# Performance work log

Measured on AMD Instinct MI355X. Metric: run time of the kernel, lower is better.

The kernel has to match this reference:

```python
import jax, jax.numpy as jnp
import numpy as np

B, L, N, C = 32, 12, 512, 2
UNITS, OUT_DIM, HORIZON, K, NUM_LAYERS = 64, 1, 12, 2, 2
M = 2 * K + 1  # 2 supports * K diffusion steps + identity


def _random_walk(adj):
    # adj: (B, N, N); D^-1 (adj + I)
    adj = adj + jnp.eye(adj.shape[1], dtype=adj.dtype)[None]
    d_inv = 1.0 / jnp.sum(adj, axis=2)
    d_inv = jnp.where(jnp.isinf(d_inv), 0.0, d_inv)
    return d_inv[:, :, None] * adj  # diag(d_inv) @ adj


def _gconv(x_in, state, supports, W, b):
    # x_in: (B, N*in), state: (B, N*units) -> (B, N*out)
    b_sz = x_in.shape[0]
    x = jnp.concatenate([x_in.reshape(b_sz, N, -1), state.reshape(b_sz, N, -1)], axis=2)
    f = x.shape[2]
    x0 = x
    xs = [x0]
    for A in supports:
        x1 = jnp.einsum('bij,bjf->bif', A, x0)
        xs.append(x1)
        for _ in range(2, K + 1):
            x2 = 2.0 * jnp.einsum('bij,bjf->bif', A, x1) - x0
            xs.append(x2)
            x1, x0 = x2, x1  # faithful to original code (x0 carries across supports)
    xcat = jnp.stack(xs, axis=0)              # (M, B, N, f)
    xcat = xcat.transpose(1, 2, 3, 0).reshape(b_sz * N, f * M)
    out = xcat @ W + b
    return out.reshape(b_sz, N * W.shape[1])


def _cell(inp, hx, supports, p):
    Wg, bg, Wc, bc = p
    gate = jax.nn.sigmoid(_gconv(inp, hx, supports, Wg, bg)).reshape(-1, N, 2 * UNITS)
    r = gate[..., :UNITS].reshape(-1, N * UNITS)
    u = gate[..., UNITS:].reshape(-1, N * UNITS)
    c = jnp.tanh(_gconv(inp, r * hx, supports, Wc, bc))
    return u * hx + (1.0 - u) * c


def setup_inputs() -> dict:
    key = jax.random.key(0)
    ks = iter(jax.random.split(key, 32))
    def nrm(shape, scale=0.1):
        return jax.random.normal(next(ks), shape, dtype=jnp.float32) * scale
    inp = {
        'history_data': jax.random.normal(next(ks), (B, L, N, C), dtype=jnp.float32),
        'hidden_states': jax.random.normal(next(ks), (B, N, 96), dtype=jnp.float32),
        'sampled_adj': jax.random.uniform(next(ks), (B, N, N), dtype=jnp.float32),
    }
    sizes = {'enc0': C + UNITS, 'enc1': 2 * UNITS, 'dec0': OUT_DIM + UNITS, 'dec1': 2 * UNITS}
    for name, isz in sizes.items():
        inp[name + '_Wg'] = nrm((isz * M, 2 * UNITS))
        inp[name + '_bg'] = jnp.ones((2 * UNITS,), jnp.float32)   # bias_start=1.0
        inp[name + '_Wc'] = nrm((isz * M, UNITS))
        inp[name + '_bc'] = jnp.zeros((UNITS,), jnp.float32)
    inp['proj_W'] = nrm((UNITS, OUT_DIM))
    inp['proj_b'] = jnp.zeros((OUT_DIM,), jnp.float32)
    inp['fc1_W'] = nrm((96, 256))
    inp['fc1_b'] = jnp.zeros((256,), jnp.float32)
    inp['fc2_W'] = nrm((256, 64))
    inp['fc2_b'] = jnp.zeros((64,), jnp.float32)
    return inp


def _forward(history_data, hidden_states, sampled_adj,
             enc0_Wg, enc0_bg, enc0_Wc, enc0_bc, enc1_Wg, enc1_bg, enc1_Wc, enc1_bc,
             dec0_Wg, dec0_bg, dec0_Wc, dec0_bc, dec1_Wg, dec1_bg, dec1_Wc, dec1_bc,
             proj_W, proj_b, fc1_W, fc1_b, fc2_W, fc2_b):
    supports = [_random_walk(sampled_adj), _random_walk(jnp.swapaxes(sampled_adj, -1, -2))]
    enc_params = [(enc0_Wg, enc0_bg, enc0_Wc, enc0_bc), (enc1_Wg, enc1_bg, enc1_Wc, enc1_bc)]
    dec_params = [(dec0_Wg, dec0_bg, dec0_Wc, dec0_bc), (dec1_Wg, dec1_bg, dec1_Wc, dec1_bc)]

    hist = jnp.transpose(history_data.reshape(B, L, N * C), (1, 0, 2))  # (L, B, N*C)

    def enc_step(h, x_t):
        out = x_t
        new_h = []
        for i, p in enumerate(enc_params):
            nh = _cell(out, h[i], supports, p)
            new_h.append(nh)
            out = nh
        return jnp.stack(new_h), None

    h0 = jnp.zeros((NUM_LAYERS, B, N * UNITS), dtype=hist.dtype)
    enc_h, _ = jax.lax.scan(enc_step, h0, hist)

    # fc_his on TSFormer hidden states, added to every encoder layer's hidden
    his = jax.nn.relu(jax.nn.relu(hidden_states @ fc1_W + fc1_b) @ fc2_W + fc2_b)  # (B, N, 64)
    enc_h = (enc_h.reshape(NUM_LAYERS, B, N, UNITS) + his[None]).reshape(NUM_LAYERS, B, N * UNITS)

    go = jnp.zeros((B, N * OUT_DIM), dtype=hist.dtype)

    def dec_step(carry, _):
        dec_in, h = carry
        out = dec_in
        new_h = []
        for i, p in enumerate(dec_params):
            nh = _cell(out, h[i], supports, p)
            new_h.append(nh)
            out = nh
        proj = (out.reshape(-1, UNITS) @ proj_W + proj_b).reshape(B, N * OUT_DIM)
        return (proj, jnp.stack(new_h)), proj

    _, outs = jax.lax.scan(dec_step, (go, enc_h), None, length=HORIZON)  # (L, B, N*OUT)
    return jnp.transpose(outs, (1, 2, 0))  # (B, N*OUT_DIM, HORIZON)


def reference(history_data, hidden_states, sampled_adj,
              enc0_Wg, enc0_bg, enc0_Wc, enc0_bc, enc1_Wg, enc1_bg, enc1_Wc, enc1_bc,
              dec0_Wg, dec0_bg, dec0_Wc, dec0_bc, dec1_Wg, dec1_bg, dec1_Wc, dec1_bc,
              proj_W, proj_b, fc1_W, fc1_b, fc2_W, fc2_b):
    return _forward(history_data, hidden_states, sampled_adj,
                    enc0_Wg, enc0_bg, enc0_Wc, enc0_bc, enc1_Wg, enc1_bg, enc1_Wc, enc1_bc,
                    dec0_Wg, dec0_bg, dec0_Wc, dec0_bc, dec1_Wg, dec1_bg, dec1_Wc, dec1_bc,
                    proj_W, proj_b, fc1_W, fc1_b, fc2_W, fc2_b)
```

## Files before the change

### kernel.cpp

```cpp
#include <hip/hip_runtime.h>
#include <stdint.h>
#include <string.h>
#include <math.h>


using bfrag = __attribute__((__ext_vector_type__(8))) short;
using accv  = __attribute__((__ext_vector_type__(4))) float;

#define DEVI static __device__ __forceinline__

DEVI float bf2f(short x) {
  union { unsigned u; float f; } v; v.u = ((unsigned)(unsigned short)x) << 16; return v.f;
}
DEVI short f2bf(float f) {
  union { float f; unsigned u; } v; v.f = f;
  unsigned r = v.u + 0x7FFFu + ((v.u >> 16) & 1u);
  return (short)(r >> 16);
}
DEVI float ldx(const void* p, long i, int f32) {
  return f32 ? ((const float*)p)[i] : bf2f(((const short*)p)[i]);
}
DEVI void gl16(const short* g, short* l) {
  __builtin_amdgcn_global_load_lds(
      (const __attribute__((address_space(1))) void*)g,
      (__attribute__((address_space(3))) void*)l, 16, 0, 0);
}
template<int N> DEVI void s_wait_vmcnt() {
  asm volatile("s_waitcnt vmcnt(%0)" :: "i"(N) : "memory");
}

struct GP {
  const short* A;  long sA;  int lda;
  const short* BT; long sBT; int ldbt;
  int K;
  short* C; long sC; int ldc;
  short* CT;
  const void* bias;
  const short* V0;
  const int* flg;
  int outDim, oshift;
  int mtiles;
  const float* h; float* hw; const float* u;
  short* xc; int inpOff;
  short* xgs; int xgsOff;
  short* xch;
  short* nxg; short* nxc;
  const void* hsrc; long hoff;
  const void* prw; const void* prb; void* dout; int tstep;
  short* xo0; short* xo1;
};

template<int EPI, int BM, int BN, int BK, int THR, int SWZ, int PIPE, int PAIR = 0>
__global__ __launch_bounds__(THR)
void gemm_k(GP pa, GP pb) {
  constexpr int W    = THR / 64;
  constexpr int WROW = BM / 32;
  constexpr int WCOL = (W / WROW < 1) ? 1 : W / WROW;
  constexpr int NT   = BN / (16 * WCOL);
  constexpr int CH   = BK / 8;
  constexpr int AI   = (BM * CH) / THR;
  constexpr int BI   = (BN * CH) / THR;
  constexpr int LD   = AI + BI;
  constexpr int TB   = (BM + BN) * BK;
  __shared__ __align__(16) short lds[PIPE*TB];
  const int tid  = threadIdx.x;
  const int w    = tid >> 6;
  const int lane = tid & 63;
  const int quad = lane >> 4, l16 = lane & 15;
  const int rowW = (w % WROW) * 32;
  const int colW = (w / WROW) * (NT * 16);
  int lay = 0;
  if constexpr (PAIR) lay = blockIdx.z;
  const GP& p = lay ? pb : pa;
  int m0, n0, bz;
  if constexpr (SWZ == 1) {
    const int blk = blockIdx.x;
    bz = blk & 31;
    const int tile = blk >> 5;
    m0 = (tile % p.mtiles) * BM;
    n0 = (tile / p.mtiles) * BN;
  } else {
    m0 = blockIdx.x * BM; n0 = blockIdx.y * BN;
    bz = PAIR ? 0 : blockIdx.z;
  }

  const short* Ab = p.A  + (long)bz * p.sA + m0 * (long)p.lda;
  const short* Bb = p.BT + (long)bz * p.sBT + n0 * (long)p.ldbt;

  accv acc[2][NT];
#pragma unroll
  for (int i = 0; i < 2; i++)
#pragma unroll
    for (int j = 0; j < NT; j++) { accv z = {0.f,0.f,0.f,0.f}; acc[i][j] = z; }

  const short* asrc[AI]; int aoff[AI];
#pragma unroll
  for (int i = 0; i < AI; i++) {
    const int s = (w*AI + i)*64 + lane;
    const int r = s / CH, c = (s % CH) ^ (r & 7);
    asrc[i] = Ab + (long)r * p.lda + c*8;
    aoff[i] = (w*AI + i)*512;
  }
  const short* bsrc[BI]; int boff[BI];
#pragma unroll
  for (int i = 0; i < BI; i++) {
    const int s = (w*BI + i)*64 + lane;
    const int r = s / CH, c = (s % CH) ^ (r & 7);
    bsrc[i] = Bb + (long)r * p.ldbt + c*8;
    boff[i] = BM*BK + (w*BI + i)*512;
  }

  const int nIter = p.K / BK;
#pragma unroll
  for (int s = 0; s < PIPE-1; ++s) {
    if (s < nIter) {
      const int kk = s * BK;
#pragma unroll
      for (int i = 0; i < AI; i++) gl16(asrc[i] + kk, &lds[s*TB + aoff[i]]);
#pragma unroll
      for (int i = 0; i < BI; i++) gl16(bsrc[i] + kk, &lds[s*TB + boff[i]]);
    }
  }

  for (int it = 0; it < nIter; ++it) {
    const int bufO = (it & (PIPE-1)) * TB;
    if (it + PIPE - 1 < nIter) {
      const int nxt = ((it + PIPE - 1) & (PIPE-1)) * TB;
      const int kk = (it + PIPE - 1) * BK;
#pragma unroll
      for (int i = 0; i < AI; i++) gl16(asrc[i] + kk, &lds[nxt + aoff[i]]);
#pragma unroll
      for (int i = 0; i < BI; i++) gl16(bsrc[i] + kk, &lds[nxt + boff[i]]);
    }
    const int rem = nIter - 1 - it;
    if (rem >= PIPE-1) { s_wait_vmcnt<(PIPE-1)*LD>(); }
    else {
      if constexpr (PIPE >= 8) { if (rem == 6) s_wait_vmcnt<6*LD>(); }
      if constexpr (PIPE >= 7) { if (rem == 5) s_wait_vmcnt<5*LD>(); }
      if constexpr (PIPE >= 6) { if (rem == 4) s_wait_vmcnt<4*LD>(); }
      if constexpr (PIPE >= 5) { if (rem == 3) s_wait_vmcnt<3*LD>(); }
      if constexpr (PIPE >= 4) { if (rem == 2) s_wait_vmcnt<2*LD>(); }
      if (rem == 1) s_wait_vmcnt<1*LD>();
      else if (rem == 0) s_wait_vmcnt<0>();
    }
    asm volatile("s_barrier" ::: "memory");
#pragma unroll
    for (int ks = 0; ks < BK; ks += 32) {
      const int ch = (ks >> 3) + quad;
      bfrag fa[2];
#pragma unroll
      for (int rt = 0; rt < 2; rt++) {
        const int ar = rowW + rt*16 + l16;
        fa[rt] = *(const bfrag*)&lds[bufO + (ar*CH + (ch ^ (ar & 7))) * 8];
      }
#pragma unroll
      for (int nt = 0; nt < NT; nt++) {
        const int br = colW + nt*16 + l16;
        bfrag fb = *(const bfrag*)&lds[bufO + BM*BK + (br*CH + (ch ^ (br & 7))) * 8];
        acc[0][nt] = __builtin_amdgcn_mfma_f32_16x16x32_bf16(fa[0], fb, acc[0][nt], 0, 0, 0);
        acc[1][nt] = __builtin_amdgcn_mfma_f32_16x16x32_bf16(fa[1], fb, acc[1][nt], 0, 0, 0);
      }
    }
    asm volatile("s_barrier" ::: "memory");
  }

  int f32 = 0;
  if constexpr (EPI == 1 || EPI == 4 || EPI == 5) f32 = *p.flg;

  if constexpr (EPI == 0 || EPI == 1 || EPI == 2) {
#pragma unroll
    for (int rt = 0; rt < 2; rt++) {
      const int rbase = m0 + rowW + rt*16 + quad*4;
#pragma unroll
      for (int nt = 0; nt < NT; nt++) {
        const int cc = n0 + colW + nt*16 + l16;
#pragma unroll
        for (int e = 0; e < 4; e++) {
          float val = acc[rt][nt][e];
          if constexpr (EPI == 1) { val += ldx(p.bias, cc, f32); val = val > 0.f ? val : 0.f; }
          p.C[(long)bz * p.sC + (long)(rbase + e) * p.ldc + cc] = f2bf(val);
        }
      }
    }
  }
  if constexpr (EPI == 2 || EPI == 3) {
    __syncthreads();
#pragma unroll
    for (int rt = 0; rt < 2; rt++)
#pragma unroll
      for (int nt = 0; nt < NT; nt++)
#pragma unroll
        for (int e = 0; e < 4; e++)
          lds[(colW + nt*16 + l16)*136 + (rowW + rt*16 + quad*4 + e)] = f2bf(acc[rt][nt][e]);
    __syncthreads();
    const int c = tid >> 2, seg = tid & 3;
    const int cG = n0 + c;
    const short* sp = &lds[c*136 + seg*32];
    long dst;
    if constexpr (EPI == 3) {
      const int m  = cG >> p.oshift;
      const int o  = cG & (p.outDim - 1);
      const int bb = m0 >> 9;
      dst = ((long)((bb * p.outDim + o) * 5 + m) << 9) + (m0 & 511) + seg*32;
    } else {
      dst = (((long)bz << 9) + cG) * 512 + m0 + seg*32;
    }
    short* dp = p.CT + dst;
    *(bfrag*)(dp)      = *(const bfrag*)(sp);
    *(bfrag*)(dp + 8)  = *(const bfrag*)(sp + 8);
    *(bfrag*)(dp + 16) = *(const bfrag*)(sp + 16);
    *(bfrag*)(dp + 24) = *(const bfrag*)(sp + 24);
  }
  if constexpr (EPI == 4) {
#pragma unroll
    for (int rt = 0; rt < 2; rt++) {
      const int nb = m0 + rowW + rt*16 + quad*4;
#pragma unroll
      for (int nt = 0; nt < NT; nt++) {
        const int o = n0 + colW + nt*16 + l16;
        const float bv = ldx(p.bias, o, f32);
#pragma unroll
        for (int e = 0; e < 4; e++) {
          const int nn = nb + e;
          float val = acc[rt][nt][e] + bv +
                      bf2f(p.V0[(long)(bz * p.outDim + o) * 2560 + nn]);
          const float s = 1.f / (1.f + __expf(-val));
          const long bn = ((long)bz << 9) + nn;
          if (o < 64) p.xc[bn*128 + p.inpOff + o] = f2bf(s * p.h[(bn << 6) + o]);
          else        p.hw[(bn << 6) + (o - 64)] = s;
        }
      }
    }
  }
  if constexpr (EPI == 5) {
    float pacc[2][4] = {};
    float pwv[NT] = {};
    const bool doproj = (p.dout != nullptr);
    if (doproj) {
#pragma unroll
      for (int nt = 0; nt < NT; nt++) pwv[nt] = ldx(p.prw, colW + nt*16 + l16, f32);
    }
#pragma unroll
    for (int rt = 0; rt < 2; rt++) {
      const int nb = m0 + rowW + rt*16 + quad*4;
#pragma unroll
      for (int nt = 0; nt < NT; nt++) {
        const int o = n0 + colW + nt*16 + l16;
        const float bv = ldx(p.bias, o, f32);
#pragma unroll
        for (int e = 0; e < 4; e++) {
          const int nn = nb + e;
          float val = acc[rt][nt][e] + bv +
                      bf2f(p.V0[(long)(bz * p.outDim + o) * 2560 + nn]);
          const float cth = tanhf(val);
          const long bn = ((long)bz << 9) + nn;
          const long idx = bn*64 + o;
          const float uo = p.u[idx];
          const float hn = uo * p.h[idx] + (1.f - uo) * cth;
          p.hw[idx] = hn;
          pacc[rt][e] += hn * pwv[nt];
          const short hb = f2bf(hn);
          if (p.xgs) p.xgs[bn*128 + p.xgsOff + o] = hb;
          if (p.nxg) { p.nxg[bn*128 + o] = hb; p.nxc[bn*128 + o] = hb; }
          if (p.hsrc != nullptr && o < 2) {
            const short hv = f2bf(ldx(p.hsrc, p.hoff + (long)bz*12288 + (long)nn*2 + o, f32));
            p.xgs[bn*128 + o] = hv;
            p.xch[bn*128 + o] = hv;
          }
        }
      }
    }
    if (doproj) {
      __syncthreads();
      float* fl = (float*)lds;
#pragma unroll
      for (int rt = 0; rt < 2; rt++)
#pragma unroll
        for (int e = 0; e < 4; e++) {
          float v = pacc[rt][e];
          v += __shfl_xor(v, 1, 16);
          v += __shfl_xor(v, 2, 16);
          v += __shfl_xor(v, 4, 16);
          v += __shfl_xor(v, 8, 16);
          if (l16 == 0) fl[(rowW + rt*16 + quad*4 + e) * WCOL + (w / WROW)] = v;
        }
      __syncthreads();
      if (tid < BM) {
        float s = ldx(p.prb, 0, f32);
#pragma unroll
        for (int g = 0; g < WCOL; g++) s += fl[tid*WCOL + g];
        const long row = ((long)bz << 9) + m0 + tid;
        if (f32) ((float*)p.dout)[row*12 + p.tstep] = s;
        else     ((short*)p.dout)[row*12 + p.tstep] = f2bf(s);
        const short ob = f2bf(s);
        p.xo0[row*128] = ob;
        p.xo1[row*128] = ob;
      }
    }
  }
}


__global__ void detect_k(const short* bg0, int* flag) {
  if (threadIdx.x == 0 && blockIdx.x == 0)
    *flag = (bg0[0] == (short)0x3F80) ? 0 : 1;
}

__global__ void rowsum_inv(const void* adj, const int* flg, float* rsi) {
  const int f32 = *flg;
  const int wid  = (blockIdx.x * 256 + threadIdx.x) >> 6;
  const int lane = threadIdx.x & 63;
  const long base = (long)wid * 512;
  float s = 0.f;
  for (int j = lane; j < 512; j += 64) s += ldx(adj, base + j, f32);
  for (int off = 32; off > 0; off >>= 1) s += __shfl_down(s, off, 64);
  if (lane == 0) rsi[wid] = 1.f / (1.f + s);
}

__global__ void colsum_inv(const void* adj, const int* flg, float* csi) {
  const int f32 = *flg;
  const int i = blockIdx.x * 256 + threadIdx.x;
  const int b = i >> 9, col = i & 511;
  const long base = (long)b * 262144 + col;
  float s = 1.f;
  for (int j = 0; j < 512; j++) s += ldx(adj, base + (long)j * 512, f32);
  csi[i] = 1.f / s;
}

__global__ __launch_bounds__(256)
void build_a(const void* adj, const int* flg, const float* rsi, const float* csi,
             short* Pbig, short* A1T, short* A2) {
  const int f32 = *flg;
  __shared__ __align__(16) float t[64 * 65];
  const int b = blockIdx.z, ti = blockIdx.x, tj = blockIdx.y;
  const int tid = threadIdx.x;
  const int r = tid >> 2, cs = (tid & 3) * 16;
  const long base = (long)b * 262144 + (long)(ti*64 + r) * 512 + tj*64 + cs;
#pragma unroll
  for (int j = 0; j < 16; j++) t[r*65 + cs + j] = ldx(adj, base + j, f32);
  __syncthreads();
  {
    const int gi = ti*64 + r;
    const float inv = rsi[b*512 + gi];
    short o[16];
#pragma unroll
    for (int j = 0; j < 16; j++) {
      const int gj = tj*64 + cs + j;
      o[j] = f2bf((t[r*65 + cs + j] + (gi == gj ? 1.f : 0.f)) * inv);
    }
    short* dp = Pbig + ((long)(b*512 + gi) << 11) + tj*64 + cs;
    bfrag v0 = {o[0],o[1],o[2],o[3],o[4],o[5],o[6],o[7]};
    bfrag v1 = {o[8],o[9],o[10],o[11],o[12],o[13],o[14],o[15]};
    *(bfrag*)dp = v0; *(bfrag*)(dp + 8) = v1;
  }
  {
    const int y = tj*64 + r;
    const float invc = csi[b*512 + y];
    short o1[16], o2[16];
#pragma unroll
    for (int j = 0; j < 16; j++) {
      const int x = ti*64 + cs + j;
      const float av = t[(cs + j)*65 + r];
      const float d = (x == y) ? 1.f : 0.f;
      o1[j] = f2bf((av + d) * rsi[b*512 + x]);
      o2[j] = f2bf((av + d) * invc);
    }
    short* d1 = A1T + ((long)(b*512 + y) << 9) + ti*64 + cs;
    short* d2 = A2  + ((long)(b*512 + y) << 9) + ti*64 + cs;
    bfrag a0 = {o1[0],o1[1],o1[2],o1[3],o1[4],o1[5],o1[6],o1[7]};
    bfrag a1 = {o1[8],o1[9],o1[10],o1[11],o1[12],o1[13],o1[14],o1[15]};
    bfrag b0 = {o2[0],o2[1],o2[2],o2[3],o2[4],o2[5],o2[6],o2[7]};
    bfrag b1 = {o2[8],o2[9],o2[10],o2[11],o2[12],o2[13],o2[14],o2[15]};
    *(bfrag*)d1 = a0; *(bfrag*)(d1 + 8) = a1;
    *(bfrag*)d2 = b0; *(bfrag*)(d2 + 8) = b1;
  }
}

__global__ void build_wcat(const void* W, const int* flg, short* WT, int f, int out) {
  const int f32 = *flg;
  const int i = blockIdx.x * 256 + threadIdx.x;
  if (i >= 5 * out * 128) return;
  const int feat = i & 127;
  const int mo = i >> 7;
  const int m = mo / out;
  const int o = mo - m * out;
  float v = 0.f;
  if (feat < f) {
    const long base = (long)feat * 5 * out;
    const float w0 = ldx(W, base + 0*out + o, f32);
    const float w1 = ldx(W, base + 1*out + o, f32);
    const float w2 = ldx(W, base + 2*out + o, f32);
    const float w3 = ldx(W, base + 3*out + o, f32);
    const float w4 = ldx(W, base + 4*out + o, f32);
    v = (m == 0) ? (w0 - w2) : (m == 1) ? (w1 - w4) : (m == 2) ? 2.f*w2
      : (m == 3) ? w3 : 2.f*w4;
  }
  WT[(long)mo * 128 + feat] = f2bf(v);
}

__global__ void build_fc1T(const void* W, const int* flg, short* WT) {
  const int f32 = *flg;
  const int i = blockIdx.x * 256 + threadIdx.x;
  const int o = i >> 7, k = i & 127;
  WT[i] = (k < 96) ? f2bf(ldx(W, (long)k*256 + o, f32)) : (short)0;
}
__global__ void build_fc2T(const void* W, const int* flg, short* WT) {
  const int f32 = *flg;
  const int i = blockIdx.x * 256 + threadIdx.x;
  const int o = i >> 8, k = i & 255;
  WT[i] = f2bf(ldx(W, (long)k*64 + o, f32));
}
__global__ void pack_hid(const void* hd, const int* flg, short* hp) {
  const int f32 = *flg;
  const int i = blockIdx.x * 256 + threadIdx.x;
  const int row = i >> 7, k = i & 127;
  hp[i] = (k < 96) ? f2bf(ldx(hd, (long)row*96 + k, f32)) : (short)0;
}

__global__ void seed_hist(const void* hist, const int* flg, short* Xg0, short* Xc0) {
  const int f32 = *flg;
  const int i = blockIdx.x * 256 + threadIdx.x;
  const int row = i >> 1, c = i & 1;
  const short v = f2bf(ldx(hist, (long)(row >> 9)*12288 + (long)(row & 511)*2 + c, f32));
  Xg0[(long)row*128 + c] = v;
  Xc0[(long)row*128 + c] = v;
}

__global__ void his_add(float* h0, float* h1, const short* his,
                        short* Xg0, short* Xc0, short* Xg1) {
  const int i = blockIdx.x * 256 + threadIdx.x;
  const int row = i >> 6, o = i & 63;
  const float v = bf2f(his[i]);
  const float a = h0[i] + v, b = h1[i] + v;
  h0[i] = a; h1[i] = b;
  Xg0[(long)row*128 + 1 + o]  = f2bf(a);
  Xg1[(long)row*128 + 64 + o] = f2bf(b);
  if (o == 0) { Xg0[(long)row*128] = 0; Xc0[(long)row*128] = 0; }
}

extern "C" void kernel_launch(void* const* d_in, const int* in_sizes, int n_in,
                              void* d_out, int out_size, void* d_ws, size_t ws_size,
                              hipStream_t stream) {
  (void)in_sizes; (void)n_in; (void)out_size;
  const void* hist   = d_in[0];
  const void* hidden = d_in[1];
  const void* adj    = d_in[2];
  const void* Wg[4] = {d_in[3], d_in[7],  d_in[11], d_in[15]};
  const void* bg[4] = {d_in[4], d_in[8],  d_in[12], d_in[16]};
  const void* Wc[4] = {d_in[5], d_in[9],  d_in[13], d_in[17]};
  const void* bc[4] = {d_in[6], d_in[10], d_in[14], d_in[18]};
  const void* projW = d_in[19];
  const void* projb = d_in[20];
  const void* fc1W  = d_in[21];
  const void* fc1b  = d_in[22];
  const void* fc2W  = d_in[23];
  const void* fc2b  = d_in[24];

  char* wp = (char*)d_ws;
  auto alloc = [&](size_t bytes) { char* r = wp; wp += (bytes + 255) & ~(size_t)255; return r; };
  short* Pbig = (short*)alloc(32ull*512*2048*2);
  float* ub   = (float*)alloc(16384ull*64*4);
  float* h0   = (float*)alloc(16384ull*64*4);
  float* h1   = (float*)alloc(16384ull*64*4);
  short* hisb = (short*)alloc(16384ull*64*2);
  short* wctg[4]; for (int i = 0; i < 4; i++) wctg[i] = (short*)alloc(640*128*2);
  short* wctc[4]; for (int i = 0; i < 4; i++) wctc[i] = (short*)alloc(320*128*2);
  float* rsi = (float*)alloc(16384*4);
  float* csi = (float*)alloc(16384*4);
  int*   flg = (int*)alloc(256);
  char* ubase = wp;
  short* hidp = (short*)ubase;
  short* mid  = (short*)(ubase + 4194304);
  short* fc1T = (short*)(ubase + 4194304 + 8388608);
  short* fc2T = (short*)(ubase + 4194304 + 8388608 + 65536);
  short* A1T  = (short*)ubase;
  short* A2   = (short*)(ubase + 16777216);
  short* P3T  = (short*)(ubase + 33554432);
  short* VTg0 = (short*)ubase;
  short* VTc0 = (short*)(ubase + 20971520);
  short* Xg0  = (short*)(ubase + 31457280);
  short* Xc0  = (short*)(ubase + 35651584);
  short* Xg1a = (short*)(ubase + 39845888);
  short* Xc1a = (short*)(ubase + 44040192);
  short* VTg1 = (short*)(ubase + 50331648);
  short* VTc1 = (short*)(ubase + 71303168);
  short* Xg1b = (short*)(ubase + 81788928);
  short* Xc1b = (short*)(ubase + 85983232);
  float* ub1  = (float*)(ubase + 90177536);
  const size_t need_serial = (size_t)(ubase - (char*)d_ws) + 50331648;
  const size_t need_pip    = (size_t)(ubase - (char*)d_ws) + 94371840;
  if (ws_size < need_serial) return;
  const bool pip = (ws_size >= need_pip);

  detect_k<<<1, 64, 0, stream>>>((const short*)bg[0], flg);
  hipMemsetAsync(h0, 0, 16384ull*64*4, stream);
  hipMemsetAsync(h1, 0, 16384ull*64*4, stream);

  const int fdim[4] = {66, 128, 65, 128};
  for (int i = 0; i < 4; i++) {
    build_wcat<<<320, 256, 0, stream>>>(Wg[i], flg, wctg[i], fdim[i], 128);
    build_wcat<<<160, 256, 0, stream>>>(Wc[i], flg, wctc[i], fdim[i], 64);
  }
  build_fc1T<<<128, 256, 0, stream>>>(fc1W, flg, fc1T);
  build_fc2T<<<64, 256, 0, stream>>>(fc2W, flg, fc2T);
  pack_hid<<<8192, 256, 0, stream>>>(hidden, flg, hidp);

  GP p;
  p = GP{}; p.A = hidp; p.lda = 128; p.BT = fc1T; p.ldbt = 128; p.K = 128;
  p.C = mid; p.ldc = 256; p.bias = fc1b; p.flg = flg;
  gemm_k<1,128,64,64,256,0,2><<<dim3(128, 4, 1), 256, 0, stream>>>(p, p);
  p = GP{}; p.A = mid; p.lda = 256; p.BT = fc2T; p.ldbt = 256; p.K = 256;
  p.C = hisb; p.ldc = 64; p.bias = fc2b; p.flg = flg;
  gemm_k<1,128,64,64,256,0,2><<<dim3(128, 1, 1), 256, 0, stream>>>(p, p);

  rowsum_inv<<<4096, 256, 0, stream>>>(adj, flg, rsi);
  colsum_inv<<<64, 256, 0, stream>>>(adj, flg, csi);
  build_a<<<dim3(8, 8, 32), 256, 0, stream>>>(adj, flg, rsi, csi, Pbig, A1T, A2);

  p = GP{}; p.A = Pbig; p.sA = 512*2048; p.lda = 2048;
  p.BT = A1T; p.sBT = 512*512; p.ldbt = 512; p.K = 512;
  p.C = Pbig + 512; p.sC = 512*2048; p.ldc = 2048; p.flg = flg;
  gemm_k<0,128,64,64,256,0,2><<<dim3(4, 8, 32), 256, 0, stream>>>(p, p);
  p = GP{}; p.A = A2; p.sA = 512*512; p.lda = 512;
  p.BT = A1T; p.sBT = 512*512; p.ldbt = 512; p.K = 512;
  p.C = Pbig + 1024; p.sC = 512*2048; p.ldc = 2048; p.CT = P3T; p.flg = flg;
  gemm_k<2,128,64,64,256,0,2><<<dim3(4, 8, 32), 256, 0, stream>>>(p, p);
  p = GP{}; p.A = A2; p.sA = 512*512; p.lda = 512;
  p.BT = P3T; p.sBT = 512*512; p.ldbt = 512; p.K = 512;
  p.C = Pbig + 1536; p.sC = 512*2048; p.ldc = 2048; p.flg = flg;
  gemm_k<0,128,64,64,256,0,2><<<dim3(4, 8, 32), 256, 0, stream>>>(p, p);

  hipMemsetAsync(Xg0, 0, 4ull*4194304, stream);
  seed_hist<<<128, 256, 0, stream>>>(hist, flg, Xg0, Xc0);

  auto run_cell = [&](int wi, int inpOff, float* hstate, short* XgL, short* XcL,
                      short* nxg, short* nxc, const void* hsrc, long hoff,
                      short* vtg, short* vtc, float* ubuf, void* dout, int tstep) {
    GP q;
    q = GP{}; q.A = XgL; q.lda = 128; q.BT = wctg[wi]; q.ldbt = 128; q.K = 128;
    q.CT = vtg; q.outDim = 128; q.oshift = 7; q.flg = flg;
    gemm_k<3,128,128,64,512,0,2><<<dim3(128, 5, 1), 512, 0, stream>>>(q, q);
    q = GP{}; q.A = Pbig; q.sA = 512*2048; q.lda = 2048;
    q.BT = vtg + 512; q.sBT = 128*2560; q.ldbt = 2560; q.K = 2048;
    q.V0 = vtg; q.outDim = 128; q.bias = bg[wi]; q.flg = flg; q.mtiles = 8;
    q.h = hstate; q.hw = ubuf; q.xc = XcL; q.inpOff = inpOff;
    gemm_k<4,64,64,64,256,1,4><<<dim3(512, 1, 1), 256, 0, stream>>>(q, q);
    q = GP{}; q.A = XcL; q.lda = 128; q.BT = wctc[wi]; q.ldbt = 128; q.K = 128;
    q.CT = vtc; q.outDim = 64; q.oshift = 6; q.flg = flg;
    gemm_k<3,128,64,64,256,0,2><<<dim3(128, 5, 1), 256, 0, stream>>>(q, q);
    q = GP{}; q.A = Pbig; q.sA = 512*2048; q.lda = 2048;
    q.BT = vtc + 512; q.sBT = 64*2560; q.ldbt = 2560; q.K = 2048;
    q.V0 = vtc; q.outDim = 64; q.bias = bc[wi]; q.flg = flg; q.mtiles = 16;
    q.h = hstate; q.hw = hstate; q.u = ubuf;
    q.xgs = XgL; q.xgsOff = inpOff; q.xch = XcL;
    q.nxg = nxg; q.nxc = nxc; q.hsrc = hsrc; q.hoff = hoff;
    q.prw = projW; q.prb = projb; q.dout = dout; q.tstep = tstep;
    q.xo0 = Xg0; q.xo1 = Xc0;
    gemm_k<5,32,64,64,256,1,4><<<dim3(512, 1, 1), 256, 0, stream>>>(q, q);
  };

  if (pip) {
    run_cell(0, 2, h0, Xg0, Xc0, Xg1a, Xc1a, hist, 1024, VTg0, VTc0, ub, nullptr, 0);
    for (int s = 1; s <= 11; s++) {
      short* XgR = ((s-1) & 1) ? Xg1b : Xg1a;
      short* XcR = ((s-1) & 1) ? Xc1b : Xc1a;
      short* XgW = (s & 1) ? Xg1b : Xg1a;
      short* XcW = (s & 1) ? Xc1b : Xc1a;
      GP qa, qb;
      qa = GP{}; qa.A = Xg0; qa.lda = 128; qa.BT = wctg[0]; qa.ldbt = 128; qa.K = 128;
      qa.CT = VTg0; qa.outDim = 128; qa.oshift = 7; qa.flg = flg;
      qb = qa; qb.A = XgR; qb.BT = wctg[1]; qb.CT = VTg1;
      gemm_k<3,128,128,64,512,0,2,1><<<dim3(128, 5, 2), 512, 0, stream>>>(qa, qb);
      qa = GP{}; qa.A = Pbig; qa.sA = 512*2048; qa.lda = 2048;
      qa.BT = VTg0 + 512; qa.sBT = 128*2560; qa.ldbt = 2560; qa.K = 2048;
      qa.V0 = VTg0; qa.outDim = 128; qa.bias = bg[0]; qa.flg = flg; qa.mtiles = 8;
      qa.h = h0; qa.hw = ub; qa.xc = Xc0; qa.inpOff = 2;
      qb = qa; qb.BT = VTg1 + 512; qb.V0 = VTg1; qb.bias = bg[1];
      qb.h = h1; qb.hw = ub1; qb.xc = XcR; qb.inpOff = 64;
      gemm_k<4,64,128,64,512,1,2,1><<<dim3(256, 1, 2), 512, 0, stream>>>(qa, qb);
      qa = GP{}; qa.A = Xc0; qa.lda = 128; qa.BT = wctc[0]; qa.ldbt = 128; qa.K = 128;
      qa.CT = VTc0; qa.outDim = 64; qa.oshift = 6; qa.flg = flg;
      qb = qa; qb.A = XcR; qb.BT = wctc[1]; qb.CT = VTc1;
      gemm_k<3,128,64,64,256,0,2,1><<<dim3(128, 5, 2), 256, 0, stream>>>(qa, qb);
      qa = GP{}; qa.A = Pbig; qa.sA = 512*2048; qa.lda = 2048;
      qa.BT = VTc0 + 512; qa.sBT = 64*2560; qa.ldbt = 2560; qa.K = 2048;
      qa.V0 = VTc0; qa.outDim = 64; qa.bias = bc[0]; qa.flg = flg; qa.mtiles = 8;
      qa.h = h0; qa.hw = h0; qa.u = ub;
      qa.xgs = Xg0; qa.xgsOff = 2; qa.xch = Xc0;
      qa.nxg = XgW; qa.nxc = XcW;
      qa.hsrc = (s < 11) ? hist : nullptr; qa.hoff = (long)(s + 1) * 1024;
      qb = qa; qb.BT = VTc1 + 512; qb.V0 = VTc1; qb.bias = bc[1];
      qb.h = h1; qb.hw = h1; qb.u = ub1;
      qb.xgs = XgW; qb.xgsOff = 64; qb.xch = nullptr;
      qb.nxg = nullptr; qb.nxc = nullptr; qb.hsrc = nullptr; qb.hoff = 0;
      gemm_k<5,64,64,64,256,1,4,1><<<dim3(256, 1, 2), 256, 0, stream>>>(qa, qb);
    }
    run_cell(1, 64, h1, Xg1b, Xc1b, nullptr, nullptr, nullptr, 0, VTg1, VTc1, ub1,
             nullptr, 0);
  } else {
    for (int t = 0; t < 12; t++) {
      run_cell(0, 2, h0, Xg0, Xc0, Xg1a, Xc1a,
               (t < 11) ? hist : nullptr, (long)(t + 1) * 1024, VTg0, VTc0, ub, nullptr, 0);
      run_cell(1, 64, h1, Xg1a, Xc1a, nullptr, nullptr, nullptr, 0, VTg0, VTc0, ub,
               nullptr, 0);
    }
  }

  his_add<<<4096, 256, 0, stream>>>(h0, h1, hisb, Xg0, Xc0, Xg1a);

  for (int t = 0; t < 12; t++) {
    run_cell(2, 1, h0, Xg0, Xc0, Xg1a, Xc1a, nullptr, 0, VTg0, VTc0, ub, nullptr, 0);
    run_cell(3, 64, h1, Xg1a, Xc1a, nullptr, nullptr, nullptr, 0, VTg0, VTc0, ub,
             d_out, t);
  }
}
```

Before: 3.145 ms.

## Fuse candidate weight projection into gate GEMM epilogue; parallelize column sums

The gate GEMM epilogue (EPI 4) now takes the freshly written r*h tile of Xc, loads the candidate weight matrix into LDS and computes the Xc·Wc projection itself, writing VTc directly. This removes the separate EPI 3 candidate projection launch each step, along with the global round-trip before it. The tile-to-block mapping is changed so that one of each pair of n-tiles owns a full row block. The column-sum kernel is also split into a partial-sum kernel with atomics plus a small inversion kernel, which gives more parallelism than the old per-column serial loop. In exchange, the epilogue does extra serialized work in only half of the gate blocks, and the atomics make the column sums nondeterministic in order.

Result: faster. 3.060 ms (-2.7%).

```diff
diff --git a/kernel.cpp b/kernel.cpp
--- a/kernel.cpp
+++ b/kernel.cpp
@@ -42,6 +42,7 @@
   int mtiles;
   const float* h; float* hw; const float* u;
   short* xc; int inpOff;
+  const short* wct; short* vtcout;
   short* xgs; int xgsOff;
   short* xch;
   short* nxg; short* nxc;
@@ -77,8 +78,12 @@
     const int blk = blockIdx.x;
     bz = blk & 31;
     const int tile = blk >> 5;
-    m0 = (tile % p.mtiles) * BM;
-    n0 = (tile / p.mtiles) * BN;
+    if (EPI == 4 && p.wct != nullptr && BN == 64) {
+      m0 = (tile >> 1) * BM; n0 = (tile & 1) * BN;
+    } else {
+      m0 = (tile % p.mtiles) * BM;
+      n0 = (tile / p.mtiles) * BN;
+    }
   } else {
     m0 = blockIdx.x * BM; n0 = blockIdx.y * BN;
     bz = PAIR ? 0 : blockIdx.z;
@@ -229,6 +234,68 @@
           if (o < 64) p.xc[bn*128 + p.inpOff + o] = f2bf(s * p.h[(bn << 6) + o]);
           else        p.hw[(bn << 6) + (o - 64)] = s;
         }
+      }
+    }
+    if (p.wct != nullptr && (BN == 128 || n0 == 0)) {
+      s_wait_vmcnt<0>();
+      __syncthreads();
+      constexpr int AG2 = 16 / W;
+      {
+        const short* xrow = p.xc + ((long)bz*512 + m0)*128;
+#pragma unroll
+        for (int i = 0; i < AG2; i++) {
+          const int s = (w*AG2 + i)*64 + lane;
+          const int r = s >> 4, c = (s & 15) ^ (r & 7);
+          gl16(xrow + (long)r*128 + c*8, &lds[(w*AG2 + i)*512]);
+        }
+      }
+      constexpr int CW2 = W / 2;
+      constexpr int NT2 = 64 / (16 * CW2);
+      const int colW2 = (w >> 1) * (NT2 * 16);
+      const int rowW2 = (w & 1) * 32;
+      for (int ncb = 0; ncb < 5; ncb++) {
+#pragma unroll
+        for (int i = 0; i < AG2; i++) {
+          const int s = (w*AG2 + i)*64 + lane;
+          const int j = s >> 4, c = (s & 15) ^ (j & 7);
+          const int cc = ncb*64 + j;
+          const int mo = (cc % 5)*64 + cc/5;
+          gl16(p.wct + (long)mo*128 + c*8, &lds[8192 + (w*AG2 + i)*512]);
+        }
+        s_wait_vmcnt<0>();
+        asm volatile("s_barrier" ::: "memory");
+        accv a2[2][NT2];
+#pragma unroll
+        for (int i2 = 0; i2 < 2; i2++)
+#pragma unroll
+          for (int j2 = 0; j2 < NT2; j2++) { accv z = {0.f,0.f,0.f,0.f}; a2[i2][j2] = z; }
+#pragma unroll
+        for (int k4 = 0; k4 < 4; k4++) {
+          bfrag fa2[2];
+#pragma unroll
+          for (int rt = 0; rt < 2; rt++) {
+            const int ar = rowW2 + rt*16 + l16;
+            fa2[rt] = *(const bfrag*)&lds[(ar*16 + ((k4*4 + quad) ^ (ar & 7)))*8];
+          }
+#pragma unroll
+          for (int nt = 0; nt < NT2; nt++) {
+            const int jb = colW2 + nt*16 + l16;
+            bfrag fb2 = *(const bfrag*)&lds[8192 + (jb*16 + ((k4*4 + quad) ^ (jb & 7)))*8];
+            a2[0][nt] = __builtin_amdgcn_mfma_f32_16x16x32_bf16(fa2[0], fb2, a2[0][nt], 0, 0, 0);
+            a2[1][nt] = __builtin_amdgcn_mfma_f32_16x16x32_bf16(fa2[1], fb2, a2[1][nt], 0, 0, 0);
+          }
+        }
+#pragma unroll
+        for (int rt = 0; rt < 2; rt++)
+#pragma unroll
+          for (int nt = 0; nt < NT2; nt++) {
+            const int cc = ncb*64 + colW2 + nt*16 + l16;
+            const long cbase = (((long)(bz*320 + cc)) << 9) + m0 + rowW2 + rt*16 + quad*4;
+#pragma unroll
+            for (int e = 0; e < 4; e++)
+              p.vtcout[cbase + e] = f2bf(a2[rt][nt][e]);
+          }
+        asm volatile("s_barrier" ::: "memory");
       }
     }
   }
@@ -317,14 +384,22 @@
   if (lane == 0) rsi[wid] = 1.f / (1.f + s);
 }
 
-__global__ void colsum_inv(const void* adj, const int* flg, float* csi) {
-  const int f32 = *flg;
+__global__ void colsum_part(const void* adj, const int* flg, float* csum) {
+  const int f32 = *flg;
+  const int b = blockIdx.x >> 4, rc = blockIdx.x & 15;
+  const int col = threadIdx.x;
+  float s0 = 0.f, s1 = 0.f;
+  const long base = (long)b * 262144 + (long)rc * 32 * 512;
+  for (int r = 0; r < 32; r++) {
+    s0 += ldx(adj, base + (long)r*512 + col, f32);
+    s1 += ldx(adj, base + (long)r*512 + col + 256, f32);
+  }
+  atomicAdd(&csum[b*512 + col], s0);
+  atomicAdd(&csum[b*512 + col + 256], s1);
+}
+__global__ void inv1p(float* v) {
   const int i = blockIdx.x * 256 + threadIdx.x;
-  const int b = i >> 9, col = i & 511;
-  const long base = (long)b * 262144 + col;
-  float s = 1.f;
-  for (int j = 0; j < 512; j++) s += ldx(adj, base + (long)j * 512, f32);
-  csi[i] = 1.f / s;
+  v[i] = 1.f / (1.f + v[i]);
 }
 
 __global__ __launch_bounds__(256)
@@ -514,7 +589,9 @@
   gemm_k<1,128,64,64,256,0,2><<<dim3(128, 1, 1), 256, 0, stream>>>(p, p);
 
   rowsum_inv<<<4096, 256, 0, stream>>>(adj, flg, rsi);
-  colsum_inv<<<64, 256, 0, stream>>>(adj, flg, csi);
+  hipMemsetAsync(csi, 0, 16384*4, stream);
+  colsum_part<<<512, 256, 0, stream>>>(adj, flg, csi);
+  inv1p<<<64, 256, 0, stream>>>(csi);
   build_a<<<dim3(8, 8, 32), 256, 0, stream>>>(adj, flg, rsi, csi, Pbig, A1T, A2);
 
   p = GP{}; p.A = Pbig; p.sA = 512*2048; p.lda = 2048;
@@ -544,10 +621,8 @@
     q.BT = vtg + 512; q.sBT = 128*2560; q.ldbt = 2560; q.K = 2048;
     q.V0 = vtg; q.outDim = 128; q.bias = bg[wi]; q.flg = flg; q.mtiles = 8;
     q.h = hstate; q.hw = ubuf; q.xc = XcL; q.inpOff = inpOff;
+    q.wct = wctc[wi]; q.vtcout = vtc;
     gemm_k<4,64,64,64,256,1,4><<<dim3(512, 1, 1), 256, 0, stream>>>(q, q);
-    q = GP{}; q.A = XcL; q.lda = 128; q.BT = wctc[wi]; q.ldbt = 128; q.K = 128;
-    q.CT = vtc; q.outDim = 64; q.oshift = 6; q.flg = flg;
-    gemm_k<3,128,64,64,256,0,2><<<dim3(128, 5, 1), 256, 0, stream>>>(q, q);
     q = GP{}; q.A = Pbig; q.sA = 512*2048; q.lda = 2048;
     q.BT = vtc + 512; q.sBT = 64*2560; q.ldbt = 2560; q.K = 2048;
     q.V0 = vtc; q.outDim = 64; q.bias = bc[wi]; q.flg = flg; q.mtiles = 16;
@@ -575,13 +650,11 @@
       qa.BT = VTg0 + 512; qa.sBT = 128*2560; qa.ldbt = 2560; qa.K = 2048;
       qa.V0 = VTg0; qa.outDim = 128; qa.bias = bg[0]; qa.flg = flg; qa.mtiles = 8;
       qa.h = h0; qa.hw = ub; qa.xc = Xc0; qa.inpOff = 2;
+      qa.wct = wctc[0]; qa.vtcout = VTc0;
       qb = qa; qb.BT = VTg1 + 512; qb.V0 = VTg1; qb.bias = bg[1];
       qb.h = h1; qb.hw = ub1; qb.xc = XcR; qb.inpOff = 64;
+      qb.wct = wctc[1]; qb.vtcout = VTc1;
       gemm_k<4,64,128,64,512,1,2,1><<<dim3(256, 1, 2), 512, 0, stream>>>(qa, qb);
-      qa = GP{}; qa.A = Xc0; qa.lda = 128; qa.BT = wctc[0]; qa.ldbt = 128; qa.K = 128;
-      qa.CT = VTc0; qa.outDim = 64; qa.oshift = 6; qa.flg = flg;
-      qb = qa; qb.A = XcR; qb.BT = wctc[1]; qb.CT = VTc1;
-      gemm_k<3,128,64,64,256,0,2,1><<<dim3(128, 5, 2), 256, 0, stream>>>(qa, qb);
       qa = GP{}; qa.A = Pbig; qa.sA = 512*2048; qa.lda = 2048;
       qa.BT = VTc0 + 512; qa.sBT = 64*2560; qa.ldbt = 2560; qa.K = 2048;
       qa.V0 = VTc0; qa.outDim = 64; qa.bias = bc[0]; qa.flg = flg; qa.mtiles = 8;
```
